# Kernel optimization log

Measured on AMD Instinct MI355X. Metric: run time of the kernel, lower is better.

Reference implementation:

```python
import jax, jax.numpy as jnp
import numpy as np

N = 8192       # number of nodes
T = 4          # number of edge types
E = 131072     # edges per type
D = 32         # edge_emb_dim
H = 4          # num_head_attentions
NEG_SLOPE = 0.2


def setup_inputs() -> dict:
    key = jax.random.key(0)
    k1, k2, k3, k4 = jax.random.split(key, 4)
    scores = jax.random.normal(k1, (N, 1), dtype=jnp.float32)
    edge_type_emb = jax.random.normal(k2, (T, D), dtype=jnp.float32)
    edge_index = jax.random.randint(k3, (T, 2, E), 0, N, dtype=jnp.int32)
    # xavier-normal-ish init for the per-head attention weights [H, D+2, 1]
    std = float(np.sqrt(2.0 / (D + 2 + 1)))
    attention_weight = jax.random.normal(k4, (H, D + 2, 1), dtype=jnp.float32) * std
    return {"scores": scores, "edge_type_emb": edge_type_emb,
            "edge_index": edge_index, "attention_weight": attention_weight}


def _head_forward(W_h, scores, edge_type_emb, src, tgt):
    # W_h: [D+2, 1]; split the concat-matmul: cat([s_src, emb, s_tgt]) @ W
    w = W_h[:, 0]
    w_src, w_emb, w_tgt = w[0], w[1:D + 1], w[D + 1]
    s = scores[:, 0]                               # [N]
    # per-edge attention logits, vectorized over edge types: [T, E]
    emb_term = edge_type_emb @ w_emb               # [T]
    vals = s[src] * w_src + s[tgt] * w_tgt + emb_term[:, None]
    # scatter-add into dense NxN (duplicates accumulate, matching += semantics)
    A = jnp.zeros((N, N), dtype=scores.dtype).at[src.ravel(), tgt.ravel()].add(vals.ravel())
    A = jnp.where(A >= 0, A, NEG_SLOPE * A)        # LeakyReLU(0.2)
    A = jax.nn.softmax(A, axis=-1)                 # dense row softmax
    return A @ scores                               # [N, 1]


def reference(scores, edge_type_emb, edge_index, attention_weight):
    src = edge_index[:, 0, :]  # [T, E]
    tgt = edge_index[:, 1, :]
    head_fn = lambda W_h: _head_forward(W_h, scores, edge_type_emb, src, tgt)
    outs = jax.vmap(head_fn)(attention_weight)      # [H, N, 1]
    return jnp.mean(outs, axis=0)                   # [N, 1]
```

## Files before the change

### kernel.cpp

```cpp
#include <hip/hip_runtime.h>
#include <stdint.h>


#define NN 8192
#define TT 4
#define EE 131072
#define DD 32
#define HH 4
#define NEG_SLOPE 0.2f

#define NB   2048
#define RPB  4
#define SEG  128
#define ABLK 256
#define EPB  2048
#define A_EPT 8
#define REGB 12288
#define EMPTY 0xFFFFFFFFu


__global__ void __launch_bounds__(256) kA(const int* __restrict__ ei,
                                          const float* __restrict__ scores,
                                          const float* __restrict__ ete,
                                          const float* __restrict__ aw,
                                          char* __restrict__ regs,
                                          float* __restrict__ f) {
    int tid = threadIdx.x;
    if (blockIdx.x == ABLK) {
        __shared__ float red[256];
        float s = 0.f;
        for (int i = tid; i < NN; i += 256) s += scores[i];
        red[tid] = s;
        __syncthreads();
        for (int off = 128; off > 0; off >>= 1) {
            if (tid < off) red[tid] += red[tid + off];
            __syncthreads();
        }
        if (tid == 0) f[0] = red[0];
        if (tid < HH) {
            f[1 + tid] = aw[tid * (DD + 2)];
            f[5 + tid] = aw[tid * (DD + 2) + DD + 1];
        }
        if (tid < HH * TT) {
            int h = tid / TT, t = tid % TT;
            float acc = 0.f;
            for (int d = 0; d < DD; ++d)
                acc += ete[t * DD + d] * aw[h * (DD + 2) + 1 + d];
            f[9 + tid] = acc;
        }
        return;
    }

    __shared__ uint32_t hist[NB];
    __shared__ uint32_t offs[NB];
    __shared__ uint32_t stage[EPB];
    __shared__ uint32_t wsum[256];

    #pragma unroll
    for (int j = 0; j < NB / 256; ++j) hist[tid + j * 256] = 0;
    __syncthreads();

    uint32_t gtid = blockIdx.x * 256u + (uint32_t)tid;
    uint32_t t  = gtid >> 14;
    uint32_t e0 = (gtid & 16383u) * A_EPT;
    const int4* sp = (const int4*)(ei + (size_t)(t * 2) * EE + e0);
    const int4* tp = (const int4*)(ei + (size_t)(t * 2 + 1) * EE + e0);

    uint32_t val[A_EPT];
    uint32_t rnk[A_EPT];
    #pragma unroll
    for (int k = 0; k < A_EPT / 4; ++k) {
        int4 s4 = sp[k];
        int4 t4 = tp[k];
        val[k*4+0] = ((uint32_t)s4.x << 15) | ((uint32_t)t4.x << 2) | t;
        val[k*4+1] = ((uint32_t)s4.y << 15) | ((uint32_t)t4.y << 2) | t;
        val[k*4+2] = ((uint32_t)s4.z << 15) | ((uint32_t)t4.z << 2) | t;
        val[k*4+3] = ((uint32_t)s4.w << 15) | ((uint32_t)t4.w << 2) | t;
    }
    #pragma unroll
    for (int k = 0; k < A_EPT; ++k)
        rnk[k] = atomicAdd(&hist[val[k] >> 17], 1u);
    __syncthreads();

    uint32_t loc[NB / 256];
    uint32_t lsum = 0;
    #pragma unroll
    for (int j = 0; j < NB / 256; ++j) {
        loc[j] = lsum;
        lsum += hist[tid * (NB / 256) + j];
    }
    wsum[tid] = lsum;
    __syncthreads();
    for (int off = 1; off < 256; off <<= 1) {
        uint32_t u = (tid >= off) ? wsum[tid - off] : 0u;
        __syncthreads();
        wsum[tid] += u;
        __syncthreads();
    }
    uint32_t base = (tid == 0) ? 0u : wsum[tid - 1];
    #pragma unroll
    for (int j = 0; j < NB / 256; ++j)
        offs[tid * (NB / 256) + j] = base + loc[j];
    __syncthreads();

    #pragma unroll
    for (int k = 0; k < A_EPT; ++k)
        stage[offs[val[k] >> 17] + rnk[k]] = val[k] & 0x1FFFFu;
    __syncthreads();

    char* reg = regs + (size_t)blockIdx.x * REGB;
    uint16_t* h16 = (uint16_t*)reg;
    uint32_t* dat = (uint32_t*)(reg + 4096);
    #pragma unroll
    for (int j = 0; j < NB / 256; ++j)
        h16[tid * (NB / 256) + j] = (uint16_t)offs[tid * (NB / 256) + j];
    #pragma unroll
    for (int j = 0; j < EPB / 256; ++j)
        dat[j * 256 + tid] = stage[j * 256 + tid];
}

__global__ void __launch_bounds__(256) kB(const float* __restrict__ scores,
                                          const char* __restrict__ regs,
                                          const float* __restrict__ f,
                                          float* __restrict__ out) {
    __shared__ uint32_t tab[RPB * SEG];
    int tid = threadIdx.x;
    tab[tid] = EMPTY;
    tab[tid + 256] = EMPTY;
    uint32_t b = blockIdx.x;

    float st = f[0];
    float wsrc[HH], wtgt[HH], em[HH * TT];
    #pragma unroll
    for (int h = 0; h < HH; ++h) { wsrc[h] = f[1 + h]; wtgt[h] = f[5 + h]; }
    #pragma unroll
    for (int k = 0; k < HH * TT; ++k) em[k] = f[9 + k];
    __syncthreads();

    const char* reg = regs + (size_t)tid * REGB;
    const uint16_t* h16 = (const uint16_t*)reg;
    const uint32_t* dat = (const uint32_t*)(reg + 4096);
    uint32_t off = h16[b];
    uint32_t nxt = (b == NB - 1) ? (uint32_t)EPB : (uint32_t)h16[b + 1];
    for (uint32_t i = off; i < nxt; ++i) {
        uint32_t v   = dat[i];
        uint32_t row = (v >> 15) & 3u;
        uint32_t tgt = (v >> 2) & 8191u;
        uint32_t tt  = v & 3u;
        uint32_t inc = 1u << (13 + 4 * tt);
        uint32_t fresh = tgt | inc;
        uint32_t pos = (tgt * 2654435761u) >> 25;
        uint32_t hb = row * SEG;
        while (true) {
            uint32_t cur = atomicCAS(&tab[hb + pos], EMPTY, fresh);
            if (cur == EMPTY) break;
            bool done = false;
            while ((cur & 0x1FFFu) == tgt) {
                uint32_t prev = atomicCAS(&tab[hb + pos], cur, cur + inc);
                if (prev == cur) { done = true; break; }
                cur = prev;
            }
            if (done) break;
            pos = (pos + 1) & (SEG - 1);
        }
    }
    __syncthreads();

    int wave = tid >> 6, lane = tid & 63;
    int r = wave;
    float si = scores[b * RPB + r];
    float num[HH] = {0.f, 0.f, 0.f, 0.f};
    float den[HH] = {0.f, 0.f, 0.f, 0.f};
    #pragma unroll
    for (int half = 0; half < 2; ++half) {
        uint32_t w = tab[r * SEG + half * 64 + lane];
        if (w != EMPTY) {
            uint32_t tgt = w & 0x1FFFu;
            float c0 = (float)((w >> 13) & 15u);
            float c1 = (float)((w >> 17) & 15u);
            float c2 = (float)((w >> 21) & 15u);
            float c3 = (float)((w >> 25) & 15u);
            float ctot = c0 + c1 + c2 + c3;
            float sj = scores[tgt];
            #pragma unroll
            for (int h = 0; h < HH; ++h) {
                float a = ctot * (si * wsrc[h] + sj * wtgt[h])
                        + c0 * em[h * 4 + 0] + c1 * em[h * 4 + 1]
                        + c2 * em[h * 4 + 2] + c3 * em[h * 4 + 3];
                a = (a >= 0.f) ? a : NEG_SLOPE * a;
                float ex = __expf(a) - 1.f;
                den[h] += ex;
                num[h] += ex * sj;
            }
        }
    }
    #pragma unroll
    for (int m = 32; m > 0; m >>= 1) {
        #pragma unroll
        for (int h = 0; h < HH; ++h) {
            num[h] += __shfl_xor(num[h], m, 64);
            den[h] += __shfl_xor(den[h], m, 64);
        }
    }
    if (lane == 0) {
        float acc = 0.f;
        #pragma unroll
        for (int h = 0; h < HH; ++h)
            acc += (st + num[h]) / ((float)NN + den[h]);
        out[b * RPB + r] = acc * (1.f / HH);
    }
}

extern "C" void kernel_launch(void* const* d_in, const int* in_sizes, int n_in,
                              void* d_out, int out_size, void* d_ws, size_t ws_size,
                              hipStream_t stream) {
    const float* scores = (const float*)d_in[0];
    const float* ete    = (const float*)d_in[1];
    const int*   ei     = (const int*)d_in[2];
    const float* aw     = (const float*)d_in[3];
    float* out = (float*)d_out;

    float* f    = (float*)d_ws;
    char*  regsp = (char*)d_ws + 256;

    kA<<<ABLK + 1, 256, 0, stream>>>(ei, scores, ete, aw, regsp, f);
    kB<<<NB, 256, 0, stream>>>(scores, regsp, f, out);
}
```

Before: 95.82 us.

## Replace per-block local bucketing with a global multi-pass counting sort of edges

```diff
diff --git a/kernel.cpp b/kernel.cpp
--- a/kernel.cpp
+++ b/kernel.cpp
@@ -9,58 +9,33 @@
 #define HH 4
 #define NEG_SLOPE 0.2f
 
-#define NB   2048
+#define NBK  2048
 #define RPB  4
 #define SEG  128
-#define ABLK 256
+#define SBLK 256
 #define EPB  2048
 #define A_EPT 8
-#define REGB 12288
 #define EMPTY 0xFFFFFFFFu
 
-
-__global__ void __launch_bounds__(256) kA(const int* __restrict__ ei,
-                                          const float* __restrict__ scores,
-                                          const float* __restrict__ ete,
-                                          const float* __restrict__ aw,
-                                          char* __restrict__ regs,
-                                          float* __restrict__ f) {
-    int tid = threadIdx.x;
-    if (blockIdx.x == ABLK) {
-        __shared__ float red[256];
-        float s = 0.f;
-        for (int i = tid; i < NN; i += 256) s += scores[i];
-        red[tid] = s;
-        __syncthreads();
-        for (int off = 128; off > 0; off >>= 1) {
-            if (tid < off) red[tid] += red[tid + off];
-            __syncthreads();
-        }
-        if (tid == 0) f[0] = red[0];
-        if (tid < HH) {
-            f[1 + tid] = aw[tid * (DD + 2)];
-            f[5 + tid] = aw[tid * (DD + 2) + DD + 1];
-        }
-        if (tid < HH * TT) {
-            int h = tid / TT, t = tid % TT;
-            float acc = 0.f;
-            for (int d = 0; d < DD; ++d)
-                acc += ete[t * DD + d] * aw[h * (DD + 2) + 1 + d];
-            f[9 + tid] = acc;
-        }
-        return;
-    }
-
-    __shared__ uint32_t hist[NB];
-    __shared__ uint32_t offs[NB];
-    __shared__ uint32_t stage[EPB];
-    __shared__ uint32_t wsum[256];
-
-    #pragma unroll
-    for (int j = 0; j < NB / 256; ++j) hist[tid + j * 256] = 0;
-    __syncthreads();
-
-    uint32_t gtid = blockIdx.x * 256u + (uint32_t)tid;
+#define OF_F    0
+#define OF_CNT  256
+#define OF_OFFS 524544
+#define OF_TOT  1573120
+#define OF_BASE 1581312
+#define OF_PACK 1589760
+#define OF_SORT 3686912
+
+__global__ void __launch_bounds__(256) kS1(const int* __restrict__ ei,
+                                           uint8_t* __restrict__ cnt,
+                                           uint32_t* __restrict__ packed) {
+    __shared__ uint32_t hist[NBK];
+    int tid = threadIdx.x;
+    #pragma unroll
+    for (int j = 0; j < NBK / 256; ++j) hist[tid + j * 256] = 0;
+    __syncthreads();
+
+    uint32_t blk = blockIdx.x;
+    uint32_t gtid = blk * 256u + (uint32_t)tid;
     uint32_t t  = gtid >> 14;
     uint32_t e0 = (gtid & 16383u) * A_EPT;
     const int4* sp = (const int4*)(ei + (size_t)(t * 2) * EE + e0);
@@ -82,14 +57,74 @@
         rnk[k] = atomicAdd(&hist[val[k] >> 17], 1u);
     __syncthreads();
 
-    uint32_t loc[NB / 256];
-    uint32_t lsum = 0;
-    #pragma unroll
-    for (int j = 0; j < NB / 256; ++j) {
-        loc[j] = lsum;
-        lsum += hist[tid * (NB / 256) + j];
-    }
-    wsum[tid] = lsum;
+    uint8_t* cb = cnt + (size_t)blk * NBK;
+    uint32_t lo = 0, hi = 0;
+    #pragma unroll
+    for (int j = 0; j < 4; ++j) lo |= (hist[tid * 8 + j] & 0xffu) << (8 * j);
+    #pragma unroll
+    for (int j = 0; j < 4; ++j) hi |= (hist[tid * 8 + 4 + j] & 0xffu) << (8 * j);
+    uint2 cpair; cpair.x = lo; cpair.y = hi;
+    ((uint2*)cb)[tid] = cpair;
+
+    uint32_t* pb = packed + (size_t)blk * EPB;
+    uint4 q0, q1;
+    q0.x = val[0] | (rnk[0] << 28); q0.y = val[1] | (rnk[1] << 28);
+    q0.z = val[2] | (rnk[2] << 28); q0.w = val[3] | (rnk[3] << 28);
+    q1.x = val[4] | (rnk[4] << 28); q1.y = val[5] | (rnk[5] << 28);
+    q1.z = val[6] | (rnk[6] << 28); q1.w = val[7] | (rnk[7] << 28);
+    ((uint4*)pb)[tid * 2]     = q0;
+    ((uint4*)pb)[tid * 2 + 1] = q1;
+}
+
+__global__ void __launch_bounds__(256) kS2(const uint8_t* __restrict__ cnt,
+                                           uint16_t* __restrict__ offs,
+                                           uint32_t* __restrict__ totals) {
+    __shared__ uint8_t  ct[SBLK * 64];
+    __shared__ uint16_t of[64 * SBLK];
+    int tid = threadIdx.x;
+    int B = blockIdx.x;
+
+    uint32_t* ct32 = (uint32_t*)ct;
+    #pragma unroll
+    for (int j = 0; j < 16; ++j) {
+        int idx = j * 256 + tid;
+        int k = idx >> 4, col = idx & 15;
+        ct32[idx] = ((const uint32_t*)(cnt + (size_t)k * NBK + B * 64))[col];
+    }
+    __syncthreads();
+
+    if (tid < 64) {
+        uint32_t run = 0;
+        for (int k = 0; k < SBLK; ++k) {
+            of[tid * SBLK + k] = (uint16_t)run;
+            run += ct[k * 64 + tid];
+        }
+        totals[B * 64 + tid] = run;
+    }
+    __syncthreads();
+
+    uint32_t* o32 = (uint32_t*)of;
+    uint32_t* d32 = (uint32_t*)(offs + (size_t)B * 64 * SBLK);
+    #pragma unroll
+    for (int j = 0; j < 32; ++j) d32[j * 256 + tid] = o32[j * 256 + tid];
+}
+
+__global__ void kS3(const uint32_t* __restrict__ totals,
+                    uint32_t* __restrict__ bases,
+                    const float* __restrict__ scores,
+                    const float* __restrict__ ete,
+                    const float* __restrict__ aw,
+                    float* __restrict__ f) {
+    __shared__ uint32_t wsum[256];
+    int tid = threadIdx.x;
+    uint32_t loc[NBK / 256];
+    uint32_t ls = 0;
+    #pragma unroll
+    for (int j = 0; j < NBK / 256; ++j) {
+        loc[j] = ls;
+        ls += totals[tid * (NBK / 256) + j];
+    }
+    wsum[tid] = ls;
     __syncthreads();
     for (int off = 1; off < 256; off <<= 1) {
         uint32_t u = (tid >= off) ? wsum[tid - off] : 0u;
@@ -99,28 +134,66 @@
     }
     uint32_t base = (tid == 0) ? 0u : wsum[tid - 1];
     #pragma unroll
-    for (int j = 0; j < NB / 256; ++j)
-        offs[tid * (NB / 256) + j] = base + loc[j];
-    __syncthreads();
-
-    #pragma unroll
-    for (int k = 0; k < A_EPT; ++k)
-        stage[offs[val[k] >> 17] + rnk[k]] = val[k] & 0x1FFFFu;
-    __syncthreads();
-
-    char* reg = regs + (size_t)blockIdx.x * REGB;
-    uint16_t* h16 = (uint16_t*)reg;
-    uint32_t* dat = (uint32_t*)(reg + 4096);
-    #pragma unroll
-    for (int j = 0; j < NB / 256; ++j)
-        h16[tid * (NB / 256) + j] = (uint16_t)offs[tid * (NB / 256) + j];
-    #pragma unroll
-    for (int j = 0; j < EPB / 256; ++j)
-        dat[j * 256 + tid] = stage[j * 256 + tid];
+    for (int j = 0; j < NBK / 256; ++j)
+        bases[tid * (NBK / 256) + j] = base + loc[j];
+    if (tid == 255) bases[NBK] = wsum[255];
+
+    __shared__ float red[256];
+    float s = 0.f;
+    for (int i = tid; i < NN; i += 256) s += scores[i];
+    red[tid] = s;
+    __syncthreads();
+    for (int off = 128; off > 0; off >>= 1) {
+        if (tid < off) red[tid] += red[tid + off];
+        __syncthreads();
+    }
+    if (tid == 0) f[0] = red[0];
+    if (tid < HH) {
+        f[1 + tid] = aw[tid * (DD + 2)];
+        f[5 + tid] = aw[tid * (DD + 2) + DD + 1];
+    }
+    if (tid < HH * TT) {
+        int h = tid / TT, t = tid % TT;
+        float acc = 0.f;
+        for (int d = 0; d < DD; ++d)
+            acc += ete[t * DD + d] * aw[h * (DD + 2) + 1 + d];
+        f[9 + tid] = acc;
+    }
+}
+
+__global__ void __launch_bounds__(256) kS4(const uint32_t* __restrict__ packed,
+                                           const uint16_t* __restrict__ offs,
+                                           const uint32_t* __restrict__ bases,
+                                           uint32_t* __restrict__ sorted) {
+    __shared__ uint32_t lbase[NBK];
+    __shared__ uint16_t lofs[NBK];
+    int tid = threadIdx.x;
+    uint32_t blk = blockIdx.x;
+    #pragma unroll
+    for (int j = 0; j < NBK / 256; ++j) {
+        int b = j * 256 + tid;
+        lbase[b] = bases[b];
+        lofs[b]  = offs[(size_t)b * SBLK + blk];
+    }
+    __syncthreads();
+    const uint4* pb = (const uint4*)(packed + (size_t)blk * EPB);
+    #pragma unroll
+    for (int q = 0; q < 2; ++q) {
+        uint4 p = pb[tid * 2 + q];
+        uint32_t w[4] = {p.x, p.y, p.z, p.w};
+        #pragma unroll
+        for (int c = 0; c < 4; ++c) {
+            uint32_t v = w[c] & 0x0FFFFFFFu;
+            uint32_t r = w[c] >> 28;
+            uint32_t b = v >> 17;
+            sorted[lbase[b] + lofs[b] + r] = v & 0x1FFFFu;
+        }
+    }
 }
 
 __global__ void __launch_bounds__(256) kB(const float* __restrict__ scores,
-                                          const char* __restrict__ regs,
+                                          const uint32_t* __restrict__ sorted,
+                                          const uint32_t* __restrict__ bases,
                                           const float* __restrict__ f,
                                           float* __restrict__ out) {
     __shared__ uint32_t tab[RPB * SEG];
@@ -135,15 +208,11 @@
     for (int h = 0; h < HH; ++h) { wsrc[h] = f[1 + h]; wtgt[h] = f[5 + h]; }
     #pragma unroll
     for (int k = 0; k < HH * TT; ++k) em[k] = f[9 + k];
-    __syncthreads();
-
-    const char* reg = regs + (size_t)tid * REGB;
-    const uint16_t* h16 = (const uint16_t*)reg;
-    const uint32_t* dat = (const uint32_t*)(reg + 4096);
-    uint32_t off = h16[b];
-    uint32_t nxt = (b == NB - 1) ? (uint32_t)EPB : (uint32_t)h16[b + 1];
-    for (uint32_t i = off; i < nxt; ++i) {
-        uint32_t v   = dat[i];
+    uint32_t lo = bases[b], hi = bases[b + 1];
+    __syncthreads();
+
+    for (uint32_t i = lo + tid; i < hi; i += 256) {
+        uint32_t v   = sorted[i];
         uint32_t row = (v >> 15) & 3u;
         uint32_t tgt = (v >> 2) & 8191u;
         uint32_t tt  = v & 3u;
@@ -220,9 +289,18 @@
     const float* aw     = (const float*)d_in[3];
     float* out = (float*)d_out;
 
-    float* f    = (float*)d_ws;
-    char*  regsp = (char*)d_ws + 256;
-
-    kA<<<ABLK + 1, 256, 0, stream>>>(ei, scores, ete, aw, regsp, f);
-    kB<<<NB, 256, 0, stream>>>(scores, regsp, f, out);
-}
+    char* ws = (char*)d_ws;
+    float*    f      = (float*)(ws + OF_F);
+    uint8_t*  cnt    = (uint8_t*)(ws + OF_CNT);
+    uint16_t* offs   = (uint16_t*)(ws + OF_OFFS);
+    uint32_t* totals = (uint32_t*)(ws + OF_TOT);
+    uint32_t* bases  = (uint32_t*)(ws + OF_BASE);
+    uint32_t* packed = (uint32_t*)(ws + OF_PACK);
+    uint32_t* sorted = (uint32_t*)(ws + OF_SORT);
+
+    kS1<<<SBLK, 256, 0, stream>>>(ei, cnt, packed);
+    kS2<<<32, 256, 0, stream>>>(cnt, offs, totals);
+    kS3<<<1, 256, 0, stream>>>(totals, bases, scores, ete, aw, f);
+    kS4<<<SBLK, 256, 0, stream>>>(packed, offs, bases, sorted);
+    kB<<<NBK, 256, 0, stream>>>(scores, sorted, bases, f, out);
+}
```

Measured after the change: 102.4 us. 1.07x slower.
